# Optimization experiments

Measured on AMD Instinct MI355X. Metric: run time of the kernel, lower is better.

## Reference

```python
import jax, jax.numpy as jnp
import numpy as np

B, S, E, H = 4, 2048, 512, 8
D = E // H


def setup_inputs() -> dict:
    key = jax.random.key(0)
    ks = jax.random.split(key, 12)
    sc = 0.02
    return {
        "x": jax.random.normal(ks[0], (B, S, E), jnp.float32),
        "edge_bias": jax.random.normal(ks[1], (B, S, S), jnp.float32),
        "attn_mask": jax.random.randint(ks[2], (B, 1, S, S), 0, 2, jnp.int32),
        "Wq": jax.random.normal(ks[3], (E, E), jnp.float32) * sc,
        "bq": jnp.zeros((E,), jnp.float32),
        "Wk": jax.random.normal(ks[4], (E, E), jnp.float32) * sc,
        "bk": jnp.zeros((E,), jnp.float32),
        "Wv": jax.random.normal(ks[5], (E, E), jnp.float32) * sc,
        "bv": jnp.zeros((E,), jnp.float32),
        "Wo": jax.random.normal(ks[6], (E, E), jnp.float32) * sc,
        "bo": jnp.zeros((E,), jnp.float32),
    }


def reference(x, edge_bias, attn_mask, Wq, bq, Wk, bk, Wv, bv, Wo, bo):
    scale = D ** -0.5
    # projections -> [B, H, S, D]
    def proj(W, b):
        return (x @ W.T + b).reshape(B, S, H, D).transpose(0, 2, 1, 3)
    q = proj(Wq, bq)
    k = proj(Wk, bk)
    v = proj(Wv, bv)
    # scores [B, H, S, S] with edge bias and mask before softmax
    scores = jnp.einsum("bhqd,bhkd->bhqk", q, k) * scale
    scores = scores + edge_bias[:, None, :, :]
    scores = jnp.where(attn_mask == 0, -jnp.inf, scores)
    probs = jax.nn.softmax(scores, axis=-1)
    out = jnp.einsum("bhqk,bhkd->bhqd", probs, v)
    out = out.transpose(0, 2, 1, 3).reshape(B, S, E)
    return out @ Wo.T + bo
```

## Files before the change

### kernel.cpp

```cpp
#include <hip/hip_runtime.h>
#include <hip/hip_bf16.h>
#include <stdint.h>

#define DEV static __device__ __forceinline__

typedef float f32x4 __attribute__((ext_vector_type(4)));
typedef int   i32x4 __attribute__((ext_vector_type(4)));
typedef unsigned short u16x4 __attribute__((ext_vector_type(4)));
typedef unsigned u32x4 __attribute__((ext_vector_type(4)));
typedef __bf16 bf16x8 __attribute__((ext_vector_type(8)));

constexpr int Bb = 4, Ss = 2048, Ee = 512, Hh = 8, Dd = 64;
constexpr float LOG2E = 1.4426950408889634f;

DEV unsigned short f2bf(float f) {
  unsigned u = __float_as_uint(f);
  u += 0x7fff + ((u >> 16) & 1);
  return (unsigned short)(u >> 16);
}
DEV float bf2f(unsigned short h) { return __uint_as_float(((unsigned)h) << 16); }

DEV unsigned cvtpk(float lo, float hi) {
  unsigned r;
  asm("v_cvt_pk_bf16_f32 %0, %1, %2" : "=v"(r) : "v"(lo), "v"(hi));
  return r;
}

DEV void gload16(const void* g, void* l) {
  __builtin_amdgcn_global_load_lds((__attribute__((address_space(1))) void*)(g),
                                   (__attribute__((address_space(3))) void*)(l), 16, 0, 0);
}

__global__ void k_cvt(const float* __restrict__ src, unsigned short* __restrict__ dst, int n4) {
  int i = blockIdx.x * 256 + threadIdx.x;
  if (i >= n4) return;
  f32x4 v = *(const f32x4*)(src + (size_t)i * 4);
  u16x4 o;
#pragma unroll
  for (int j = 0; j < 4; ++j) o[j] = f2bf(v[j]);
  *(u16x4*)(dst + (size_t)i * 4) = o;
}

__global__ void k_mb(const float* __restrict__ bias, const int* __restrict__ mask,
                     unsigned short* __restrict__ mb, int n4) {
  int i = blockIdx.x * 256 + threadIdx.x;
  if (i >= n4) return;
  f32x4 v = *(const f32x4*)(bias + (size_t)i * 4);
  i32x4 m = *(const i32x4*)(mask + (size_t)i * 4);
  u16x4 o;
  const unsigned short NEG = f2bf(-1e38f * LOG2E);
#pragma unroll
  for (int j = 0; j < 4; ++j) o[j] = m[j] ? f2bf(v[j] * LOG2E) : NEG;
  *(u16x4*)(mb + (size_t)i * 4) = o;
}

template <int MODE>
__global__ __launch_bounds__(256) void k_gemm(
    const unsigned short* __restrict__ A, const unsigned short* __restrict__ Bw,
    const float* __restrict__ b0, const float* __restrict__ b1, const float* __restrict__ b2,
    unsigned short* __restrict__ oq, unsigned short* __restrict__ ok,
    unsigned short* __restrict__ ovt, float* __restrict__ of32) {
  __shared__ unsigned short Asl[128 * 32];
  __shared__ unsigned short Bsl[128 * 32];
  const int tid = threadIdx.x;
  const int wave = tid >> 6, lane = tid & 63;
  const int l15 = lane & 15, lg = lane >> 4;
  const int brow = blockIdx.x, bcol = blockIdx.y;
  const int wm = (wave >> 1) * 64, wn = (wave & 1) * 64;

  f32x4 acc[4][4] = {};

  for (int k0 = 0; k0 < 512; k0 += 32) {
    __syncthreads();
#pragma unroll
    for (int rnd = 0; rnd < 2; ++rnd) {
      int vid = rnd * 256 + tid;
      int r = vid >> 2, c = vid & 3;
      gload16(A + (size_t)(brow * 128 + r) * 512 + k0 + c * 8,
              Asl + (size_t)(rnd * 256 + wave * 64) * 8);
      gload16(Bw + (size_t)(bcol * 128 + r) * 512 + k0 + c * 8,
              Bsl + (size_t)(rnd * 256 + wave * 64) * 8);
    }
    __syncthreads();
    bf16x8 af[4], bfr[4];
#pragma unroll
    for (int m = 0; m < 4; ++m) af[m] = *(const bf16x8*)(Asl + (wm + m * 16 + l15) * 32 + lg * 8);
#pragma unroll
    for (int n = 0; n < 4; ++n) bfr[n] = *(const bf16x8*)(Bsl + (wn + n * 16 + l15) * 32 + lg * 8);
#pragma unroll
    for (int m = 0; m < 4; ++m)
#pragma unroll
      for (int n = 0; n < 4; ++n)
        acc[m][n] = __builtin_amdgcn_mfma_f32_16x16x32_bf16(af[m], bfr[n], acc[m][n], 0, 0, 0);
  }

  if (MODE == 0) {
    const int Nbase = bcol * 128;
    const int mat = Nbase >> 9;
    const int colb = Nbase & 511;
    const float* bp = (mat == 0) ? b0 : ((mat == 1) ? b1 : b2);
#pragma unroll
    for (int m = 0; m < 4; ++m)
#pragma unroll
      for (int n = 0; n < 4; ++n) {
        const int col = colb + wn + n * 16 + l15;
        const int h = col >> 6, d = col & 63;
        const float bv = bp[col];
#pragma unroll
        for (int j = 0; j < 4; ++j) {
          const int M = brow * 128 + wm + m * 16 + lg * 4 + j;
          const int b = M >> 11, s = M & 2047;
          float outv = acc[m][n][j] + bv;
          if (mat == 0) outv *= 0.125f * LOG2E;
          const unsigned short hv = f2bf(outv);
          if (mat == 0)
            oq[(((size_t)(b * Hh + h)) * Ss + s) * Dd + d] = hv;
          else if (mat == 1)
            ok[(((size_t)(b * Hh + h)) * Ss + s) * Dd + d] = hv;
          else
            ovt[(((size_t)(b * Hh + h)) * Dd + d) * Ss + s] = hv;
        }
      }
  } else {
#pragma unroll
    for (int m = 0; m < 4; ++m)
#pragma unroll
      for (int n = 0; n < 4; ++n) {
        const int col = bcol * 128 + wn + n * 16 + l15;
        const float bv = b0[col];
#pragma unroll
        for (int j = 0; j < 4; ++j) {
          const int M = brow * 128 + wm + m * 16 + lg * 4 + j;
          of32[(size_t)M * 512 + col] = acc[m][n][j] + bv;
        }
      }
  }
}

__global__ __launch_bounds__(256, 4) void k_attn(
    const unsigned short* __restrict__ q, const unsigned short* __restrict__ k,
    const unsigned short* __restrict__ vt, const unsigned short* __restrict__ mb,
    unsigned short* __restrict__ att) {
  __shared__ unsigned short Ksl[2][4096];
  __shared__ unsigned short Vsl[2][4096];
  const int tid = threadIdx.x;
  const int wave = tid >> 6, lane = tid & 63;
  const int l15 = lane & 15, lg = lane >> 4;
  const int qt = blockIdx.x, bh = blockIdx.y;
  const int b = bh >> 3, h = bh & 7;
  const size_t qkb = (size_t)bh * Ss * Dd;
  const size_t vtbase = (size_t)bh * Dd * Ss;
  const int q0 = qt * 64 + wave * 16;
  const int qrow = q0 + l15;

  const int addrA = (l15 + 32 * (lg & 1)) * 4;
  const int addrB = addrA + 64;
  const bool hi = (lg >> 1) != 0;

  bf16x8 qf[2];
#pragma unroll
  for (int ks = 0; ks < 2; ++ks)
    qf[ks] = *(const bf16x8*)(q + qkb + (size_t)qrow * Dd + ks * 32 + lg * 8);

  const size_t mbrow = ((size_t)b * Ss + qrow) * Ss;

  f32x4 accO[4] = {};
  float mrow = -INFINITY, lrow = 0.f;

  auto stage = [&](int buf, int t) {
    const int key0 = t * 64;
#pragma unroll
    for (int rnd = 0; rnd < 2; ++rnd) {
      int v2 = rnd * 256 + tid;
      int ks = v2 >> 8, r = (v2 >> 2) & 63, c = v2 & 3;
      gload16(k + qkb + (size_t)(key0 + r) * Dd + ks * 32 + c * 8,
              &Ksl[buf][(rnd * 256 + wave * 64) * 8]);
    }
#pragma unroll
    for (int rnd = 0; rnd < 2; ++rnd) {
      int v2 = rnd * 256 + tid;
      int ks = v2 >> 8, r = (v2 >> 2) & 63, c = v2 & 3;
      gload16(vt + vtbase + (size_t)r * Ss + key0 + ks * 32 + c * 8,
              &Vsl[buf][(rnd * 256 + wave * 64) * 8]);
    }
  };

  stage(0, 0);
  u16x4 bvc[4], bvn[4];
#pragma unroll
  for (int m = 0; m < 4; ++m) bvc[m] = *(const u16x4*)(mb + mbrow + m * 16 + lg * 4);

  for (int t = 0; t < 32; ++t) {
    const int cur = t & 1;
    __syncthreads();

    if (t < 31) {
      stage(cur ^ 1, t + 1);
#pragma unroll
      for (int m = 0; m < 4; ++m)
        bvn[m] = *(const u16x4*)(mb + mbrow + (t + 1) * 64 + m * 16 + lg * 4);
    }

    f32x4 sc[4] = {};
#pragma unroll
    for (int ks = 0; ks < 2; ++ks) {
      bf16x8 kfm[4];
#pragma unroll
      for (int m = 0; m < 4; ++m)
        kfm[m] = *(const bf16x8*)(&Ksl[cur][ks * 2048 + (m * 16 + l15) * 32 + lg * 8]);
#pragma unroll
      for (int m = 0; m < 4; ++m)
        sc[m] = __builtin_amdgcn_mfma_f32_16x16x32_bf16(kfm[m], qf[ks], sc[m], 0, 0, 0);
    }

    float pm = -INFINITY;
#pragma unroll
    for (int m = 0; m < 4; ++m)
#pragma unroll
      for (int j = 0; j < 4; ++j) {
        sc[m][j] += bf2f(bvc[m][j]);
        pm = fmaxf(pm, sc[m][j]);
      }
    pm = fmaxf(pm, __shfl_xor(pm, 16));
    pm = fmaxf(pm, __shfl_xor(pm, 32));
    const float mnew = fmaxf(mrow, pm);
    if (!__all(pm <= mrow)) {
      const float c = exp2f(mrow - mnew);
      lrow *= c;
#pragma unroll
      for (int n = 0; n < 4; ++n) accO[n] *= c;
    }
    mrow = mnew;
    float rs = 0.f;
#pragma unroll
    for (int m = 0; m < 4; ++m)
#pragma unroll
      for (int j = 0; j < 4; ++j) {
        const float p = exp2f(sc[m][j] - mnew);
        sc[m][j] = p;
        rs += p;
      }
    rs += __shfl_xor(rs, 16);
    rs += __shfl_xor(rs, 32);
    lrow += rs;

    unsigned pk[4][2];
#pragma unroll
    for (int m = 0; m < 4; ++m) {
      pk[m][0] = cvtpk(sc[m][0], sc[m][1]);
      pk[m][1] = cvtpk(sc[m][2], sc[m][3]);
    }

#pragma unroll
    for (int ks2 = 0; ks2 < 2; ++ks2) {
      bf16x8 va[4];
#pragma unroll
      for (int n = 0; n < 4; ++n)
        va[n] = *(const bf16x8*)(&Vsl[cur][ks2 * 2048 + (n * 16 + l15) * 32 + lg * 8]);
      const int mlo = 2 * ks2, mhi = 2 * ks2 + 1;
      unsigned lo0 = __builtin_amdgcn_ds_bpermute(addrA, pk[mlo][0]);
      unsigned hi0 = __builtin_amdgcn_ds_bpermute(addrA, pk[mhi][0]);
      unsigned lo1 = __builtin_amdgcn_ds_bpermute(addrA, pk[mlo][1]);
      unsigned hi1 = __builtin_amdgcn_ds_bpermute(addrA, pk[mhi][1]);
      unsigned lo2 = __builtin_amdgcn_ds_bpermute(addrB, pk[mlo][0]);
      unsigned hi2 = __builtin_amdgcn_ds_bpermute(addrB, pk[mhi][0]);
      unsigned lo3 = __builtin_amdgcn_ds_bpermute(addrB, pk[mlo][1]);
      unsigned hi3 = __builtin_amdgcn_ds_bpermute(addrB, pk[mhi][1]);
      u32x4 wv;
      wv[0] = hi ? hi0 : lo0;
      wv[1] = hi ? hi1 : lo1;
      wv[2] = hi ? hi2 : lo2;
      wv[3] = hi ? hi3 : lo3;
      const bf16x8 pB = __builtin_bit_cast(bf16x8, wv);
#pragma unroll
      for (int n = 0; n < 4; ++n)
        accO[n] = __builtin_amdgcn_mfma_f32_16x16x32_bf16(va[n], pB, accO[n], 0, 0, 0);
    }

#pragma unroll
    for (int m = 0; m < 4; ++m) bvc[m] = bvn[m];
  }

  const float invl = 1.0f / lrow;
#pragma unroll
  for (int n = 0; n < 4; ++n) {
    u16x4 o;
#pragma unroll
    for (int j = 0; j < 4; ++j) o[j] = f2bf(accO[n][j] * invl);
    *(u16x4*)(att + ((size_t)b * Ss + qrow) * Ee + h * Dd + n * 16 + lg * 4) = o;
  }
}

extern "C" void kernel_launch(void* const* d_in, const int* in_sizes, int n_in,
                              void* d_out, int out_size, void* d_ws, size_t ws_size,
                              hipStream_t stream) {
  const float* x  = (const float*)d_in[0];
  const float* eb = (const float*)d_in[1];
  const int*   am = (const int*)d_in[2];
  const float* Wq = (const float*)d_in[3];
  const float* bq = (const float*)d_in[4];
  const float* Wk = (const float*)d_in[5];
  const float* bk = (const float*)d_in[6];
  const float* Wv = (const float*)d_in[7];
  const float* bv = (const float*)d_in[8];
  const float* Wo = (const float*)d_in[9];
  const float* bo = (const float*)d_in[10];
  float* out = (float*)d_out;

  unsigned short* xb   = (unsigned short*)d_ws;
  unsigned short* wqkv = xb + (size_t)8192 * 512;
  unsigned short* wo   = wqkv + (size_t)1536 * 512;
  unsigned short* qb   = wo + (size_t)512 * 512;
  unsigned short* kb   = qb + (size_t)Bb * Hh * Ss * Dd;
  unsigned short* vtb  = kb + (size_t)Bb * Hh * Ss * Dd;
  unsigned short* attb = vtb + (size_t)Bb * Hh * Ss * Dd;
  unsigned short* mbb  = attb + (size_t)8192 * 512;

  k_cvt<<<4096, 256, 0, stream>>>(x, xb, 8192 * 512 / 4);
  k_cvt<<<256, 256, 0, stream>>>(Wq, wqkv, 512 * 512 / 4);
  k_cvt<<<256, 256, 0, stream>>>(Wk, wqkv + (size_t)512 * 512, 512 * 512 / 4);
  k_cvt<<<256, 256, 0, stream>>>(Wv, wqkv + (size_t)1024 * 512, 512 * 512 / 4);
  k_cvt<<<256, 256, 0, stream>>>(Wo, wo, 512 * 512 / 4);
  k_mb<<<16384, 256, 0, stream>>>(eb, am, mbb, Bb * Ss * Ss / 4);

  dim3 blk(256);
  dim3 g1(64, 12);
  k_gemm<0><<<g1, blk, 0, stream>>>(xb, wqkv, bq, bk, bv, qb, kb, vtb, nullptr);
  dim3 g2(32, 32);
  k_attn<<<g2, blk, 0, stream>>>(qb, kb, vtb, mbb, attb);
  dim3 g3(64, 4);
  k_gemm<1><<<g3, blk, 0, stream>>>(attb, wo, bo, nullptr, nullptr, nullptr, nullptr, nullptr, out);
}
```

Measured before the change: 181.1 us.

## Fuse edge-bias and mask preprocessing into attention kernel, rowsum via MFMA

Removes the separate pass that turned fp32 edge bias and the int mask into a bf16 log2-scaled tensor. The attention kernel now reads the raw fp32 bias and int mask directly and double-buffers them in registers. The masked bias becomes the initial accumulator of the QK MFMA, which drops a separate add. The softmax row sum is taken with an extra MFMA against a ones vector instead of shuffle reductions. This removes one full-size intermediate write and read, at the cost of each head re-reading 8 bytes per score element instead of 2, which relies on cache reuse across heads, and of higher register pressure.

```diff
diff --git a/kernel.cpp b/kernel.cpp
--- a/kernel.cpp
+++ b/kernel.cpp
@@ -39,19 +39,6 @@
 #pragma unroll
   for (int j = 0; j < 4; ++j) o[j] = f2bf(v[j]);
   *(u16x4*)(dst + (size_t)i * 4) = o;
-}
-
-__global__ void k_mb(const float* __restrict__ bias, const int* __restrict__ mask,
-                     unsigned short* __restrict__ mb, int n4) {
-  int i = blockIdx.x * 256 + threadIdx.x;
-  if (i >= n4) return;
-  f32x4 v = *(const f32x4*)(bias + (size_t)i * 4);
-  i32x4 m = *(const i32x4*)(mask + (size_t)i * 4);
-  u16x4 o;
-  const unsigned short NEG = f2bf(-1e38f * LOG2E);
-#pragma unroll
-  for (int j = 0; j < 4; ++j) o[j] = m[j] ? f2bf(v[j] * LOG2E) : NEG;
-  *(u16x4*)(mb + (size_t)i * 4) = o;
 }
 
 template <int MODE>
@@ -139,8 +126,8 @@
 
 __global__ __launch_bounds__(256, 4) void k_attn(
     const unsigned short* __restrict__ q, const unsigned short* __restrict__ k,
-    const unsigned short* __restrict__ vt, const unsigned short* __restrict__ mb,
-    unsigned short* __restrict__ att) {
+    const unsigned short* __restrict__ vt, const float* __restrict__ eb,
+    const int* __restrict__ am, unsigned short* __restrict__ att) {
   __shared__ unsigned short Ksl[2][4096];
   __shared__ unsigned short Vsl[2][4096];
   const int tid = threadIdx.x;
@@ -162,10 +149,15 @@
   for (int ks = 0; ks < 2; ++ks)
     qf[ks] = *(const bf16x8*)(q + qkb + (size_t)qrow * Dd + ks * 32 + lg * 8);
 
-  const size_t mbrow = ((size_t)b * Ss + qrow) * Ss;
+  const size_t ebrow = ((size_t)b * Ss + qrow) * Ss + lg * 4;
+
+  const unsigned one2 = 0x3F803F80u;
+  u32x4 ow; ow[0] = one2; ow[1] = one2; ow[2] = one2; ow[3] = one2;
+  const bf16x8 onesv = __builtin_bit_cast(bf16x8, ow);
 
   f32x4 accO[4] = {};
-  float mrow = -INFINITY, lrow = 0.f;
+  f32x4 accL = {};
+  float mrow = -INFINITY;
 
   auto stage = [&](int buf, int t) {
     const int key0 = t * 64;
@@ -186,63 +178,74 @@
   };
 
   stage(0, 0);
-  u16x4 bvc[4], bvn[4];
-#pragma unroll
-  for (int m = 0; m < 4; ++m) bvc[m] = *(const u16x4*)(mb + mbrow + m * 16 + lg * 4);
-
-  for (int t = 0; t < 32; ++t) {
+  f32x4 bvfA[4], bvfB[4];
+  i32x4 bvmA[4], bvmB[4];
+#pragma unroll
+  for (int m = 0; m < 4; ++m) {
+    bvfA[m] = *(const f32x4*)(eb + ebrow + m * 16);
+    bvmA[m] = *(const i32x4*)(am + ebrow + m * 16);
+  }
+
+  auto body = [&](int t, f32x4 (&bvfC)[4], i32x4 (&bvmC)[4],
+                  f32x4 (&bvfN)[4], i32x4 (&bvmN)[4]) {
     const int cur = t & 1;
     __syncthreads();
 
     if (t < 31) {
       stage(cur ^ 1, t + 1);
+      const size_t nb = ebrow + (size_t)(t + 1) * 64;
+#pragma unroll
+      for (int m = 0; m < 4; ++m) {
+        bvfN[m] = *(const f32x4*)(eb + nb + m * 16);
+        bvmN[m] = *(const i32x4*)(am + nb + m * 16);
+      }
+    }
+
+    f32x4 binit[4];
+#pragma unroll
+    for (int m = 0; m < 4; ++m)
+#pragma unroll
+      for (int j = 0; j < 4; ++j)
+        binit[m][j] = bvmC[m][j] ? bvfC[m][j] * LOG2E : -1e38f;
+
+    f32x4 sc[4];
+    {
+      bf16x8 kfm[4];
 #pragma unroll
       for (int m = 0; m < 4; ++m)
-        bvn[m] = *(const u16x4*)(mb + mbrow + (t + 1) * 64 + m * 16 + lg * 4);
-    }
-
-    f32x4 sc[4] = {};
-#pragma unroll
-    for (int ks = 0; ks < 2; ++ks) {
-      bf16x8 kfm[4];
+        kfm[m] = *(const bf16x8*)(&Ksl[cur][(m * 16 + l15) * 32 + lg * 8]);
 #pragma unroll
       for (int m = 0; m < 4; ++m)
-        kfm[m] = *(const bf16x8*)(&Ksl[cur][ks * 2048 + (m * 16 + l15) * 32 + lg * 8]);
+        sc[m] = __builtin_amdgcn_mfma_f32_16x16x32_bf16(kfm[m], qf[0], binit[m], 0, 0, 0);
 #pragma unroll
       for (int m = 0; m < 4; ++m)
-        sc[m] = __builtin_amdgcn_mfma_f32_16x16x32_bf16(kfm[m], qf[ks], sc[m], 0, 0, 0);
-    }
-
-    float pm = -INFINITY;
-#pragma unroll
-    for (int m = 0; m < 4; ++m)
-#pragma unroll
-      for (int j = 0; j < 4; ++j) {
-        sc[m][j] += bf2f(bvc[m][j]);
-        pm = fmaxf(pm, sc[m][j]);
-      }
+        kfm[m] = *(const bf16x8*)(&Ksl[cur][2048 + (m * 16 + l15) * 32 + lg * 8]);
+#pragma unroll
+      for (int m = 0; m < 4; ++m)
+        sc[m] = __builtin_amdgcn_mfma_f32_16x16x32_bf16(kfm[m], qf[1], sc[m], 0, 0, 0);
+    }
+
+    float mm[4];
+#pragma unroll
+    for (int m = 0; m < 4; ++m)
+      mm[m] = fmaxf(fmaxf(fmaxf(sc[m][0], sc[m][1]), sc[m][2]), sc[m][3]);
+    float pm = fmaxf(fmaxf(fmaxf(mm[0], mm[1]), mm[2]), mm[3]);
     pm = fmaxf(pm, __shfl_xor(pm, 16));
     pm = fmaxf(pm, __shfl_xor(pm, 32));
     const float mnew = fmaxf(mrow, pm);
     if (!__all(pm <= mrow)) {
       const float c = exp2f(mrow - mnew);
-      lrow *= c;
 #pragma unroll
       for (int n = 0; n < 4; ++n) accO[n] *= c;
+      accL *= c;
     }
     mrow = mnew;
-    float rs = 0.f;
-#pragma unroll
-    for (int m = 0; m < 4; ++m)
-#pragma unroll
-      for (int j = 0; j < 4; ++j) {
-        const float p = exp2f(sc[m][j] - mnew);
-        sc[m][j] = p;
-        rs += p;
-      }
-    rs += __shfl_xor(rs, 16);
-    rs += __shfl_xor(rs, 32);
-    lrow += rs;
+
+#pragma unroll
+    for (int m = 0; m < 4; ++m)
+#pragma unroll
+      for (int j = 0; j < 4; ++j)
+        sc[m][j] = exp2f(sc[m][j] - mnew);
 
     unsigned pk[4][2];
 #pragma unroll
@@ -275,13 +278,16 @@
 #pragma unroll
       for (int n = 0; n < 4; ++n)
         accO[n] = __builtin_amdgcn_mfma_f32_16x16x32_bf16(va[n], pB, accO[n], 0, 0, 0);
-    }
-
-#pragma unroll
-    for (int m = 0; m < 4; ++m) bvc[m] = bvn[m];
-  }
-
-  const float invl = 1.0f / lrow;
+      accL = __builtin_amdgcn_mfma_f32_16x16x32_bf16(onesv, pB, accL, 0, 0, 0);
+    }
+  };
+
+  for (int t2 = 0; t2 < 16; ++t2) {
+    body(2 * t2, bvfA, bvmA, bvfB, bvmB);
+    body(2 * t2 + 1, bvfB, bvmB, bvfA, bvmA);
+  }
+
+  const float invl = 1.0f / accL[0];
 #pragma unroll
   for (int n = 0; n < 4; ++n) {
     u16x4 o;
@@ -314,20 +320,18 @@
   unsigned short* kb   = qb + (size_t)Bb * Hh * Ss * Dd;
   unsigned short* vtb  = kb + (size_t)Bb * Hh * Ss * Dd;
   unsigned short* attb = vtb + (size_t)Bb * Hh * Ss * Dd;
-  unsigned short* mbb  = attb + (size_t)8192 * 512;
 
   k_cvt<<<4096, 256, 0, stream>>>(x, xb, 8192 * 512 / 4);
   k_cvt<<<256, 256, 0, stream>>>(Wq, wqkv, 512 * 512 / 4);
   k_cvt<<<256, 256, 0, stream>>>(Wk, wqkv + (size_t)512 * 512, 512 * 512 / 4);
   k_cvt<<<256, 256, 0, stream>>>(Wv, wqkv + (size_t)1024 * 512, 512 * 512 / 4);
   k_cvt<<<256, 256, 0, stream>>>(Wo, wo, 512 * 512 / 4);
-  k_mb<<<16384, 256, 0, stream>>>(eb, am, mbb, Bb * Ss * Ss / 4);
 
   dim3 blk(256);
   dim3 g1(64, 12);
   k_gemm<0><<<g1, blk, 0, stream>>>(xb, wqkv, bq, bk, bv, qb, kb, vtb, nullptr);
   dim3 g2(32, 32);
-  k_attn<<<g2, blk, 0, stream>>>(qb, kb, vtb, mbb, attb);
+  k_attn<<<g2, blk, 0, stream>>>(qb, kb, vtb, eb, am, attb);
   dim3 g3(64, 4);
   k_gemm<1><<<g3, blk, 0, stream>>>(attb, wo, bo, nullptr, nullptr, nullptr, nullptr, nullptr, out);
 }
```

New measurement: 241.5 us. +33.4%, slower.
